# Performance work log

Measured on AMD Instinct MI355X. Metric: run time of the kernel, lower is better.

Reference implementation:

```python
import jax, jax.numpy as jnp
import numpy as np

B, T, C = 64, 384, 256
NH, NKV = 4, 2
HD = C // NH            # 64
NREP = NH // NKV        # 2
NE, TOPK = 8, 2
HID = int(8 / 3 * C)    # 682
EPS_RMS = 1e-6


def _rope_tables(t_len):
    inv_freq = 1.0 / (10000.0 ** (np.arange(0, HD, 2, dtype=np.float32) / HD))
    t = np.arange(t_len, dtype=np.float32)
    freqs = np.outer(t, inv_freq)                      # [T, HD/2]
    emb = np.concatenate([freqs, freqs], axis=-1)      # [T, HD]
    return jnp.asarray(np.cos(emb)), jnp.asarray(np.sin(emb))


def _rotate_half(x):
    h = x.shape[-1] // 2
    return jnp.concatenate([-x[..., h:], x[..., :h]], axis=-1)


def _rmsnorm(v, w):
    return v * jax.lax.rsqrt(jnp.mean(v * v, axis=-1, keepdims=True) + EPS_RMS) * w


def setup_inputs() -> dict:
    key = jax.random.key(0)
    ks = jax.random.split(key, 10)
    s = lambda k, shape: (jax.random.normal(k, shape, jnp.float32) * 0.02)
    return {
        "x": jax.random.normal(ks[0], (B, T, C), jnp.float32),
        "ln1_w": jnp.ones((C,), jnp.float32),
        "ln2_w": jnp.ones((C,), jnp.float32),
        "wq": s(ks[1], (NH * HD, C)),
        "wk": s(ks[2], (NKV * HD, C)),
        "wv": s(ks[3], (NKV * HD, C)),
        "wo": s(ks[4], (C, C)),
        "router_w": s(ks[5], (NE, C)),
        "w1": s(ks[6], (NE, HID, C)),
        "w2": s(ks[7], (NE, C, HID)),
        "w3": s(ks[8], (NE, HID, C)),
    }


def reference(x, ln1_w, ln2_w, wq, wk, wv, wo, router_w, w1, w2, w3):
    Bx, Tx, Cx = x.shape
    # --- attention sub-block ---
    h = _rmsnorm(x, ln1_w)
    q = (h @ wq.T).reshape(Bx, Tx, NH, HD).transpose(0, 2, 1, 3)    # [B,H,T,D]
    k = (h @ wk.T).reshape(Bx, Tx, NKV, HD).transpose(0, 2, 1, 3)   # [B,KV,T,D]
    v = (h @ wv.T).reshape(Bx, Tx, NKV, HD).transpose(0, 2, 1, 3)
    cos, sin = _rope_tables(Tx)
    cos, sin = cos[None, None], sin[None, None]
    q = q * cos + _rotate_half(q) * sin
    k = k * cos + _rotate_half(k) * sin
    k = jnp.repeat(k, NREP, axis=1)   # GQA: expand kv heads
    v = jnp.repeat(v, NREP, axis=1)
    scores = jnp.einsum('bhtd,bhsd->bhts', q, k) / jnp.sqrt(jnp.float32(HD))
    causal = jnp.tril(jnp.ones((Tx, Tx), dtype=bool))
    scores = jnp.where(causal[None, None], scores, jnp.float32(-1e30))
    att = jax.nn.softmax(scores, axis=-1)
    y = jnp.einsum('bhts,bhsd->bhtd', att, v).transpose(0, 2, 1, 3).reshape(Bx, Tx, Cx)
    x = x + y @ wo.T

    # --- MoE sub-block ---
    flat = _rmsnorm(x, ln2_w).reshape(-1, Cx)                  # [N, C]
    probs = jax.nn.softmax(flat @ router_w.T, axis=-1)         # [N, NE]
    tp, ti = jax.lax.top_k(probs, TOPK)
    tp = tp / (jnp.sum(tp, axis=-1, keepdims=True) + 1e-9)
    # per-token per-expert combine weight (0 if not selected)
    weights = jnp.sum(tp[..., None] * jax.nn.one_hot(ti, NE, dtype=flat.dtype), axis=1)  # [N, NE]
    out = jnp.zeros_like(flat)
    for e in range(NE):  # small fixed expert count
        hh = jax.nn.silu(flat @ w1[e].T) * (flat @ w3[e].T)
        out = out + weights[:, e:e + 1] * (hh @ w2[e].T)
    return x + out.reshape(Bx, Tx, Cx)
```

## Files before the change

kernel.cpp:

```cpp
#include <hip/hip_runtime.h>
#include <hip/hip_bf16.h>
#include <math.h>

typedef unsigned short u16t;
typedef __bf16 bf16x8 __attribute__((ext_vector_type(8)));
typedef float f32x4 __attribute__((ext_vector_type(4)));

#define NBATCH 64
#define NT 384
#define NC 256
#define NHID 682
#define NHIDP 704
#define NTOK (NBATCH * NT)
#define NSLOT (2 * NTOK + 1024)

#define SB0 196
#define SB1 (SB0 + 512)
#define SB2 (SB1 + 256)
#define SB3 (SB2 + 5632)
#define SB4 (SB3 + 5632)
#define SB5 (SB4 + 48)
#define SB6 (SB5 + NTOK / 4)

static __device__ __forceinline__ float bf2f(u16t u) { return __uint_as_float(((unsigned int)u) << 16); }
static __device__ __forceinline__ u16t f2bf(float f) { return __builtin_bit_cast(u16t, __float2bfloat16(f)); }

static __device__ __forceinline__ void gload16(const void* gp, void* lp) {
  __builtin_amdgcn_global_load_lds((const __attribute__((address_space(1))) void*)gp,
                                   (__attribute__((address_space(3))) void*)lp, 16, 0, 0);
}

static __device__ __forceinline__ void pipe_barrier_full() {
  asm volatile("s_waitcnt vmcnt(0) lgkmcnt(0)" ::: "memory");
  __builtin_amdgcn_s_barrier();
  asm volatile("" ::: "memory");
}


__global__ __launch_bounds__(256) void k_setup(const float* __restrict__ wq, const float* __restrict__ wk,
                                               const float* __restrict__ wv, const float* __restrict__ wo,
                                               const float* __restrict__ w1, const float* __restrict__ w2,
                                               const float* __restrict__ w3,
                                               const float* __restrict__ x, const float* __restrict__ ln1w,
                                               int* __restrict__ tok, float* __restrict__ tokw,
                                               int* __restrict__ ctrl,
                                               u16t* __restrict__ wqkvb, u16t* __restrict__ wob,
                                               u16t* __restrict__ w1p, u16t* __restrict__ w3p,
                                               u16t* __restrict__ w2p, float* __restrict__ rtab,
                                               u16t* __restrict__ h) {
  int blk = blockIdx.x, t = threadIdx.x;
  if (blk < SB0) {
    int i = blk * 256 + t;
    tok[i] = -1; tokw[i] = 0.f;
    if (blk == 0 && t < 64) ctrl[t] = 0;
  } else if (blk < SB1) {
    int i = (blk - SB0) * 256 + t;
    int row = i >> 8, col = i & 255;
    float s = (row < 256) ? wq[(size_t)row * 256 + col]
            : (row < 384) ? wk[(size_t)(row - 256) * 256 + col]
                          : wv[(size_t)(row - 384) * 256 + col];
    wqkvb[i] = f2bf(s);
  } else if (blk < SB2) {
    int i = (blk - SB1) * 256 + t;
    wob[i] = f2bf(wo[i]);
  } else if (blk < SB3) {
    int idx = (blk - SB2) * 256 + t;
    int kcol = idx & 255; int tmp = idx >> 8; int nrow = tmp % NHIDP; int e = tmp / NHIDP;
    if (nrow < NHID) {
      size_t src = ((size_t)e * NHID + nrow) * NC + kcol;
      w1p[idx] = f2bf(w1[src]); w3p[idx] = f2bf(w3[src]);
    } else { w1p[idx] = 0; w3p[idx] = 0; }
  } else if (blk < SB4) {
    int idx = (blk - SB3) * 256 + t;
    int kcol = idx % NHIDP; int tmp = idx / NHIDP; int nrow = tmp & 255; int e = tmp >> 8;
    w2p[idx] = (kcol < NHID) ? f2bf(w2[((size_t)e * NC + nrow) * NHID + kcol]) : (u16t)0;
  } else if (blk < SB5) {
    int i = (blk - SB4) * 256 + t;
    int tt = i >> 5, d = i & 31;
    float ang = (float)tt * powf(10000.f, -(float)d * (1.f / 32.f));
    float s, c; sincosf(ang, &s, &c);
    ((float2*)rtab)[i] = make_float2(c, s);
  } else {
    int w = t >> 6, l = t & 63;
    int n = (blk - SB5) * 4 + w;
    const float* xr = x + (size_t)n * NC;
    float4 xa = *(const float4*)(xr + l * 4);
    float ssq = xa.x * xa.x + xa.y * xa.y + xa.z * xa.z + xa.w * xa.w;
    for (int d = 1; d < 64; d <<= 1) ssq += __shfl_xor(ssq, d, 64);
    float rs = rsqrtf(ssq * (1.f / 256.f) + 1e-6f);
    float4 wa = *(const float4*)(ln1w + l * 4);
    ushort4 o;
    o.x = f2bf(xa.x * rs * wa.x);
    o.y = f2bf(xa.y * rs * wa.y);
    o.z = f2bf(xa.z * rs * wa.z);
    o.w = f2bf(xa.w * rs * wa.w);
    *(ushort4*)(h + (size_t)n * NC + l * 4) = o;
  }
}

__global__ __launch_bounds__(256) void k_rms_router(const float* __restrict__ xin,
                                                    const float* __restrict__ wg,
                                                    const float* __restrict__ rw,
                                                    u16t* __restrict__ flat,
                                                    int* __restrict__ eidx,
                                                    float* __restrict__ ew) {
  int w = threadIdx.x >> 6, l = threadIdx.x & 63;
  int n = blockIdx.x * 4 + w;
  const float* xr = xin + (size_t)n * NC;
  float4 xa = *(const float4*)(xr + l * 4);
  float ssq = xa.x * xa.x + xa.y * xa.y + xa.z * xa.z + xa.w * xa.w;
  for (int d = 1; d < 64; d <<= 1) ssq += __shfl_xor(ssq, d, 64);
  float rs = rsqrtf(ssq * (1.f / 256.f) + 1e-6f);
  float4 wa = *(const float4*)(wg + l * 4);
  float n0 = xa.x * rs * wa.x, n1 = xa.y * rs * wa.y;
  float n2 = xa.z * rs * wa.z, n3 = xa.w * rs * wa.w;
  ushort4 o; o.x = f2bf(n0); o.y = f2bf(n1); o.z = f2bf(n2); o.w = f2bf(n3);
  *(ushort4*)(flat + (size_t)n * NC + l * 4) = o;
  float acc[8];
  for (int e = 0; e < 8; e++) {
    float4 ra = *(const float4*)(rw + (size_t)e * NC + l * 4);
    acc[e] = n0 * ra.x + n1 * ra.y + n2 * ra.z + n3 * ra.w;
  }
  for (int e = 0; e < 8; e++)
    for (int d = 1; d < 64; d <<= 1) acc[e] += __shfl_xor(acc[e], d, 64);
  if (l == 0) {
    float mx = acc[0];
    for (int e = 1; e < 8; e++) mx = fmaxf(mx, acc[e]);
    float p[8], sum = 0.f;
    for (int e = 0; e < 8; e++) { p[e] = __expf(acc[e] - mx); sum += p[e]; }
    float inv = 1.f / sum;
    for (int e = 0; e < 8; e++) p[e] *= inv;
    int i0 = 0; float b0 = p[0];
    for (int e = 1; e < 8; e++) if (p[e] > b0) { b0 = p[e]; i0 = e; }
    int i1 = -1; float b1 = -1.f;
    for (int e = 0; e < 8; e++) if (e != i0 && p[e] > b1) { b1 = p[e]; i1 = e; }
    float s2 = 1.f / (b0 + b1 + 1e-9f);
    eidx[n * 2] = i0; eidx[n * 2 + 1] = i1;
    ew[n * 2] = b0 * s2; ew[n * 2 + 1] = b1 * s2;
  }
}

__global__ __launch_bounds__(256) void k_hist(const int* __restrict__ eidx, int* __restrict__ ctrl) {
  int* cnt = ctrl; int* offs = ctrl + 8; int* cursor = ctrl + 20; int* done = ctrl + 32;
  __shared__ int lh[8];
  if (threadIdx.x < 8) lh[threadIdx.x] = 0;
  __syncthreads();
  int base = blockIdx.x * 1024 + threadIdx.x;
  for (int i = 0; i < 4; i++) atomicAdd(&lh[eidx[base + i * 256]], 1);
  __syncthreads();
  if (threadIdx.x < 8) {
    atomicAdd(&cnt[threadIdx.x], lh[threadIdx.x]);
    __threadfence();
  }
  __syncthreads();
  if (threadIdx.x == 0) {
    int prev = atomicAdd(done, 1);
    if (prev == 47) {
      int off = 0;
      for (int e = 0; e < 8; e++) {
        int c_ = atomicAdd(&cnt[e], 0);
        offs[e] = off; cursor[e] = off;
        off += ((c_ + 127) >> 7) << 7;
      }
      offs[8] = off;
    }
  }
}

__global__ __launch_bounds__(256) void k_gemm_qkv(const u16t* __restrict__ A,
                                                  const u16t* __restrict__ Bw,
                                                  const float* __restrict__ rtab,
                                                  u16t* __restrict__ qkv) {
  __shared__ __align__(16) u16t sA[2][128 * 64];
  __shared__ __align__(16) u16t sB[2][128 * 64];
  int t = threadIdx.x;
  int m0 = blockIdx.y * 128, n0 = blockIdx.x * 128;
  int w = t >> 6, l = t & 63, quad = l >> 4, lq = l & 15;
  int wm = (w >> 1) * 64, wn = (w & 1) * 64;
  const u16t* aP[4]; const u16t* bP[4];
  for (int i = 0; i < 4; i++) {
    int c = i * 256 + t; int r = c >> 3; int g = (c & 7) ^ (r & 7);
    aP[i] = A + (size_t)(m0 + r) * NC + g * 8;
    bP[i] = Bw + (size_t)(n0 + r) * NC + g * 8;
  }
  auto stage = [&](int p, int k0) {
    for (int i = 0; i < 4; i++) {
      gload16(aP[i] + k0, sA[p] + (size_t)(i * 256 + t) * 8);
      gload16(bP[i] + k0, sB[p] + (size_t)(i * 256 + t) * 8);
    }
  };
  const f32x4 fz = {0.f, 0.f, 0.f, 0.f};
  f32x4 acc[4][4];
  for (int i = 0; i < 4; i++) for (int j = 0; j < 4; j++) acc[i][j] = fz;
  stage(0, 0);
  pipe_barrier_full();
  for (int kb = 0; kb < 4; kb++) {
    int p = kb & 1;
    if (kb < 3) stage(p ^ 1, (kb + 1) << 6);
    for (int kk = 0; kk < 2; kk++) {
      int gq = kk * 4 + quad;
      bf16x8 af[4], bf[4];
      for (int mi = 0; mi < 4; mi++) { int row = wm + mi * 16 + lq; af[mi] = *(const bf16x8*)(sA[p] + (row * 8 + (gq ^ (row & 7))) * 8); }
      for (int ni = 0; ni < 4; ni++) { int row = wn + ni * 16 + lq; bf[ni] = *(const bf16x8*)(sB[p] + (row * 8 + (gq ^ (row & 7))) * 8); }
      for (int mi = 0; mi < 4; mi++)
        for (int ni = 0; ni < 4; ni++)
          acc[mi][ni] = __builtin_amdgcn_mfma_f32_16x16x32_bf16(af[mi], bf[ni], acc[mi][ni], 0, 0, 0);
    }
    if (kb < 3) pipe_barrier_full();
  }
  int cb = (n0 + wn) >> 6;
  const float2* rt = (const float2*)rtab;
  for (int mi = 0; mi < 4; mi++)
    for (int r = 0; r < 4; r++) {
      int gm = m0 + wm + mi * 16 + quad * 4 + r;
      u16t* orow = qkv + (size_t)gm * 512 + n0 + wn;
      if (cb < 6) {
        int tt = gm % NT;
        for (int ni = 0; ni < 2; ni++) {
          int d = ni * 16 + lq;
          float2 cs = rt[tt * 32 + d];
          float x1 = acc[mi][ni][r], x2 = acc[mi][ni + 2][r];
          orow[d] = f2bf(x1 * cs.x - x2 * cs.y);
          orow[d + 32] = f2bf(x2 * cs.x + x1 * cs.y);
        }
      } else {
        for (int ni = 0; ni < 4; ni++) orow[ni * 16 + lq] = f2bf(acc[mi][ni][r]);
      }
    }
}

__global__ __launch_bounds__(256) void k_gemm_wo(const u16t* __restrict__ A,
                                                 const u16t* __restrict__ Bw,
                                                 const float* __restrict__ xin,
                                                 float* __restrict__ xo) {
  __shared__ __align__(16) u16t sA[2][128 * 64];
  __shared__ __align__(16) u16t sB[2][128 * 64];
  int t = threadIdx.x;
  int m0 = blockIdx.y * 128, n0 = blockIdx.x * 128;
  int w = t >> 6, l = t & 63, quad = l >> 4, lq = l & 15;
  int wm = (w >> 1) * 64, wn = (w & 1) * 64;
  const u16t* aP[4]; const u16t* bP[4];
  for (int i = 0; i < 4; i++) {
    int c = i * 256 + t; int r = c >> 3; int g = (c & 7) ^ (r & 7);
    aP[i] = A + (size_t)(m0 + r) * NC + g * 8;
    bP[i] = Bw + (size_t)(n0 + r) * NC + g * 8;
  }
  auto stage = [&](int p, int k0) {
    for (int i = 0; i < 4; i++) {
      gload16(aP[i] + k0, sA[p] + (size_t)(i * 256 + t) * 8);
      gload16(bP[i] + k0, sB[p] + (size_t)(i * 256 + t) * 8);
    }
  };
  const f32x4 fz = {0.f, 0.f, 0.f, 0.f};
  f32x4 acc[4][4];
  for (int i = 0; i < 4; i++) for (int j = 0; j < 4; j++) acc[i][j] = fz;
  stage(0, 0);
  pipe_barrier_full();
  for (int kb = 0; kb < 4; kb++) {
    int p = kb & 1;
    if (kb < 3) stage(p ^ 1, (kb + 1) << 6);
    for (int kk = 0; kk < 2; kk++) {
      int gq = kk * 4 + quad;
      bf16x8 af[4], bf[4];
      for (int mi = 0; mi < 4; mi++) { int row = wm + mi * 16 + lq; af[mi] = *(const bf16x8*)(sA[p] + (row * 8 + (gq ^ (row & 7))) * 8); }
      for (int ni = 0; ni < 4; ni++) { int row = wn + ni * 16 + lq; bf[ni] = *(const bf16x8*)(sB[p] + (row * 8 + (gq ^ (row & 7))) * 8); }
      for (int mi = 0; mi < 4; mi++)
        for (int ni = 0; ni < 4; ni++)
          acc[mi][ni] = __builtin_amdgcn_mfma_f32_16x16x32_bf16(af[mi], bf[ni], acc[mi][ni], 0, 0, 0);
    }
    if (kb < 3) pipe_barrier_full();
  }
  for (int mi = 0; mi < 4; mi++)
    for (int ni = 0; ni < 4; ni++) {
      int gn = n0 + wn + ni * 16 + lq;
      for (int r = 0; r < 4; r++) {
        int gm = m0 + wm + mi * 16 + quad * 4 + r;
        xo[(size_t)gm * NC + gn] = acc[mi][ni][r] + xin[(size_t)gm * NC + gn];
      }
    }
}

__global__ __launch_bounds__(256) void k_attn(const u16t* __restrict__ qkv,
                                              u16t* __restrict__ y) {
  __shared__ __align__(16) u16t sK[2][64 * 64];
  __shared__ __align__(16) u16t sVT[2][64 * 64];
  __shared__ __align__(16) u16t sP[4 * 32 * 64];
  int qt = blockIdx.x, h = blockIdx.y, b = blockIdx.z;
  int kvh = h >> 1;
  int t = threadIdx.x, w = t >> 6, l = t & 63, quad = l >> 4, lq = l & 15;
  int tb = qt * 128 + w * 32;
  bf16x8 qf[2][2];
  for (int mi = 0; mi < 2; mi++)
    for (int kk = 0; kk < 2; kk++)
      qf[mi][kk] = *(const bf16x8*)(qkv + ((size_t)(b * NT + tb + mi * 16 + lq)) * 512 + h * 64 + kk * 32 + quad * 8);
  const f32x4 fz = {0.f, 0.f, 0.f, 0.f};
  f32x4 accO[2][4];
  float mrow[2][4], lrow[2][4];
  for (int mi = 0; mi < 2; mi++)
    for (int ni = 0; ni < 4; ni++) accO[mi][ni] = fz;
  for (int mi = 0; mi < 2; mi++)
    for (int r = 0; r < 4; r++) { mrow[mi][r] = -1e30f; lrow[mi][r] = 0.f; }
  u16t* myP = sP + w * 2048;
  int nkt = (qt + 1) * 2;
  ushort4 vr0[2], vr1[2];
  auto stageK = [&](int p, int kt) {
    int s0 = kt * 64;
    for (int i = 0; i < 2; i++) {
      int c = i * 256 + t; int s = c >> 3; int g = (c & 7) ^ (s & 7);
      gload16(qkv + ((size_t)(b * NT + s0 + s)) * 512 + 256 + kvh * 64 + g * 8, sK[p] + (size_t)c * 8);
    }
  };
  auto vload = [&](int kt) {
    int s0 = kt * 64;
    for (int i = 0; i < 2; i++) {
      int pI = i * 256 + t; int s = pI & 63; int n0 = (pI >> 6) * 8;
      const u16t* vp = qkv + ((size_t)(b * NT + s0 + s)) * 512 + 384 + kvh * 64 + n0;
      vr0[i] = *(const ushort4*)vp; vr1[i] = *(const ushort4*)(vp + 4);
    }
  };
  auto vstore = [&](int p) {
    for (int i = 0; i < 2; i++) {
      int pI = i * 256 + t; int s = pI & 63; int n0 = (pI >> 6) * 8;
      u16t vv[8] = {vr0[i].x, vr0[i].y, vr0[i].z, vr0[i].w, vr1[i].x, vr1[i].y, vr1[i].z, vr1[i].w};
      for (int j = 0; j < 8; j++) {
        int nn = n0 + j;
        sVT[p][(nn * 8 + ((s >> 3) ^ (nn & 7))) * 8 + (s & 7)] = vv[j];
      }
    }
  };
  stageK(0, 0); vload(0); vstore(0);
  pipe_barrier_full();
  for (int kt = 0; kt < nkt; kt++) {
    int p = kt & 1;
    int s0 = kt * 64;
    bool more = (kt + 1 < nkt);
    if (more) { stageK(p ^ 1, kt + 1); vload(kt + 1); }
    if (s0 <= tb + 31) {
      f32x4 accS[2][4];
      for (int mi = 0; mi < 2; mi++) for (int ni = 0; ni < 4; ni++) accS[mi][ni] = fz;
      for (int kk = 0; kk < 2; kk++) {
        int gq = kk * 4 + quad;
        bf16x8 kf[4];
        for (int ni = 0; ni < 4; ni++) { int row = ni * 16 + lq; kf[ni] = *(const bf16x8*)(sK[p] + (row * 8 + (gq ^ (row & 7))) * 8); }
        for (int mi = 0; mi < 2; mi++)
          for (int ni = 0; ni < 4; ni++)
            accS[mi][ni] = __builtin_amdgcn_mfma_f32_16x16x32_bf16(qf[mi][kk], kf[ni], accS[mi][ni], 0, 0, 0);
      }
      for (int mi = 0; mi < 2; mi++) {
        float alpha[4];
        for (int r = 0; r < 4; r++) {
          int trow = tb + mi * 16 + quad * 4 + r;
          float mx = -1e30f;
          for (int ni = 0; ni < 4; ni++) {
            int ss = s0 + ni * 16 + lq;
            float sv = accS[mi][ni][r] * 0.125f;
            sv = (ss > trow) ? -1e30f : sv;
            accS[mi][ni][r] = sv;
            mx = fmaxf(mx, sv);
          }
          for (int d = 1; d < 16; d <<= 1) mx = fmaxf(mx, __shfl_xor(mx, d, 64));
          float mnew = fmaxf(mrow[mi][r], mx);
          float al = __expf(mrow[mi][r] - mnew);
          float rsum = 0.f;
          for (int ni = 0; ni < 4; ni++) {
            float p2 = __expf(accS[mi][ni][r] - mnew);
            accS[mi][ni][r] = p2;
            rsum += p2;
          }
          for (int d = 1; d < 16; d <<= 1) rsum += __shfl_xor(rsum, d, 64);
          lrow[mi][r] = lrow[mi][r] * al + rsum;
          mrow[mi][r] = mnew;
          alpha[r] = al;
        }
        for (int ni = 0; ni < 4; ni++)
          for (int r = 0; r < 4; r++) accO[mi][ni][r] *= alpha[r];
        for (int ni = 0; ni < 4; ni++) {
          int cc = ni * 16 + lq;
          for (int r = 0; r < 4; r++) {
            int row = mi * 16 + quad * 4 + r;
            myP[((cc >> 3) * 32 + row) * 8 + (cc & 7)] = f2bf(accS[mi][ni][r]);
          }
        }
      }
      asm volatile("s_waitcnt lgkmcnt(0)" ::: "memory");
      for (int kk = 0; kk < 2; kk++) {
        int gq = kk * 4 + quad;
        bf16x8 pf[2], vf[4];
        for (int mi = 0; mi < 2; mi++) { int row = mi * 16 + lq; pf[mi] = *(const bf16x8*)(myP + (gq * 32 + row) * 8); }
        for (int ni = 0; ni < 4; ni++) { int row = ni * 16 + lq; vf[ni] = *(const bf16x8*)(sVT[p] + (row * 8 + (gq ^ (row & 7))) * 8); }
        for (int mi = 0; mi < 2; mi++)
          for (int ni = 0; ni < 4; ni++)
            accO[mi][ni] = __builtin_amdgcn_mfma_f32_16x16x32_bf16(pf[mi], vf[ni], accO[mi][ni], 0, 0, 0);
      }
    }
    if (more) {
      vstore(p ^ 1);
      pipe_barrier_full();
    }
  }
  for (int mi = 0; mi < 2; mi++)
    for (int r = 0; r < 4; r++) {
      int trow = tb + mi * 16 + quad * 4 + r;
      float inv = 1.f / lrow[mi][r];
      for (int ni = 0; ni < 4; ni++) {
        int d = ni * 16 + lq;
        y[((size_t)(b * NT + trow)) * NC + h * 64 + d] = f2bf(accO[mi][ni][r] * inv);
      }
    }
}

__global__ __launch_bounds__(256) void k_scatter(const int* __restrict__ eidx, const float* __restrict__ ew,
                                                 int* __restrict__ cursor, int* __restrict__ tok,
                                                 float* __restrict__ tokw, int* __restrict__ t2s) {
  __shared__ int lcnt[8], lbase[8];
  if (threadIdx.x < 8) lcnt[threadIdx.x] = 0;
  __syncthreads();
  int n = blockIdx.x * 256 + threadIdx.x;
  int e0 = eidx[n * 2], e1 = eidx[n * 2 + 1];
  int p0 = atomicAdd(&lcnt[e0], 1);
  int p1 = atomicAdd(&lcnt[e1], 1);
  __syncthreads();
  if (threadIdx.x < 8) lbase[threadIdx.x] = atomicAdd(&cursor[threadIdx.x], lcnt[threadIdx.x]);
  __syncthreads();
  int g0 = lbase[e0] + p0, g1 = lbase[e1] + p1;
  tok[g0] = n; tokw[g0] = ew[n * 2];
  tok[g1] = n; tokw[g1] = ew[n * 2 + 1];
  t2s[n * 2] = g0; t2s[n * 2 + 1] = g1;
}

__global__ __launch_bounds__(256) void k_moe_e1(const u16t* __restrict__ flat,
                                                const u16t* __restrict__ w1p,
                                                const u16t* __restrict__ w3p,
                                                const int* __restrict__ offs,
                                                const int* __restrict__ tok,
                                                u16t* __restrict__ hh) {
  __shared__ __align__(16) u16t sA[128 * 64];
  __shared__ __align__(16) u16t sB1[64 * 64];
  __shared__ __align__(16) u16t sB3[64 * 64];
  int t = threadIdx.x;
  int bid = blockIdx.x;
  int work = (bid & 7) * 539 + (bid >> 3);
  int sb = work / 11;
  int slot0 = sb * 128, n0 = (work - sb * 11) * 64;
  int e = 7;
  for (int i = 0; i < 8; i++) { if (slot0 < offs[i + 1]) { e = i; break; } }
  const u16t* B1 = w1p + (size_t)e * NHIDP * NC;
  const u16t* B3 = w3p + (size_t)e * NHIDP * NC;
  int w = t >> 6, l = t & 63, quad = l >> 4, lq = l & 15;
  int wm = (w >> 1) * 64, wn = (w & 1) * 32;
  const u16t* aP[4]; const u16t* b1P[2]; const u16t* b3P[2];
  for (int i = 0; i < 4; i++) {
    int c = i * 256 + t; int r = c >> 3; int g = (c & 7) ^ (r & 7);
    int tk = tok[slot0 + r]; int row = (tk < 0) ? 0 : tk;
    aP[i] = flat + (size_t)row * NC + g * 8;
  }
  for (int i = 0; i < 2; i++) {
    int c = i * 256 + t; int r = c >> 3; int g = (c & 7) ^ (r & 7);
    b1P[i] = B1 + (size_t)(n0 + r) * NC + g * 8;
    b3P[i] = B3 + (size_t)(n0 + r) * NC + g * 8;
  }
  const f32x4 fz = {0.f, 0.f, 0.f, 0.f};
  f32x4 a1[4][2], a3[4][2];
  for (int i = 0; i < 4; i++) for (int j = 0; j < 2; j++) { a1[i][j] = fz; a3[i][j] = fz; }
  for (int kb = 0; kb < 4; kb++) {
    int k0 = kb << 6;
    for (int i = 0; i < 4; i++)
      gload16(aP[i] + k0, sA + (size_t)(i * 256 + t) * 8);
    for (int i = 0; i < 2; i++) {
      gload16(b1P[i] + k0, sB1 + (size_t)(i * 256 + t) * 8);
      gload16(b3P[i] + k0, sB3 + (size_t)(i * 256 + t) * 8);
    }
    __syncthreads();
    for (int kk = 0; kk < 2; kk++) {
      int gq = kk * 4 + quad;
      bf16x8 af[4], b1f[2], b3f[2];
      for (int mi = 0; mi < 4; mi++) { int row = wm + mi * 16 + lq; af[mi] = *(const bf16x8*)(sA + (row * 8 + (gq ^ (row & 7))) * 8); }
      for (int ni = 0; ni < 2; ni++) {
        int row = wn + ni * 16 + lq;
        b1f[ni] = *(const bf16x8*)(sB1 + (row * 8 + (gq ^ (row & 7))) * 8);
        b3f[ni] = *(const bf16x8*)(sB3 + (row * 8 + (gq ^ (row & 7))) * 8);
      }
      for (int mi = 0; mi < 4; mi++)
        for (int ni = 0; ni < 2; ni++) {
          a1[mi][ni] = __builtin_amdgcn_mfma_f32_16x16x32_bf16(af[mi], b1f[ni], a1[mi][ni], 0, 0, 0);
          a3[mi][ni] = __builtin_amdgcn_mfma_f32_16x16x32_bf16(af[mi], b3f[ni], a3[mi][ni], 0, 0, 0);
        }
    }
    __syncthreads();
  }
  for (int mi = 0; mi < 4; mi++)
    for (int ni = 0; ni < 2; ni++) {
      int gn = n0 + wn + ni * 16 + lq;
      for (int r = 0; r < 4; r++) {
        int slot = slot0 + wm + mi * 16 + quad * 4 + r;
        float v1 = a1[mi][ni][r], v3 = a3[mi][ni][r];
        float hv = v1 / (1.f + __expf(-v1)) * v3;
        hh[(size_t)slot * NHIDP + gn] = f2bf(hv);
      }
    }
}

__global__ __launch_bounds__(256) void k_moe_e2(const u16t* __restrict__ hh,
                                                const u16t* __restrict__ w2p,
                                                const int* __restrict__ offs,
                                                const float* __restrict__ tokw,
                                                u16t* __restrict__ eo) {
  __shared__ __align__(16) u16t sA[128 * 64];
  __shared__ __align__(16) u16t sB[128 * 64];
  int t = threadIdx.x;
  int bid = blockIdx.x;
  int work = (bid & 7) * 98 + (bid >> 3);
  int slot0 = (work >> 1) * 128, n0 = (work & 1) * 128;
  int e = 7;
  for (int i = 0; i < 8; i++) { if (slot0 < offs[i + 1]) { e = i; break; } }
  const u16t* Bw = w2p + (size_t)e * NC * NHIDP;
  int w = t >> 6, l = t & 63, quad = l >> 4, lq = l & 15;
  int wm = (w >> 1) * 64, wn = (w & 1) * 64;
  const u16t* aP[4]; const u16t* bP[4];
  for (int i = 0; i < 4; i++) {
    int c = i * 256 + t; int r = c >> 3; int g = (c & 7) ^ (r & 7);
    aP[i] = hh + (size_t)(slot0 + r) * NHIDP + g * 8;
    bP[i] = Bw + (size_t)(n0 + r) * NHIDP + g * 8;
  }
  const f32x4 fz = {0.f, 0.f, 0.f, 0.f};
  f32x4 acc[4][4];
  for (int i = 0; i < 4; i++) for (int j = 0; j < 4; j++) acc[i][j] = fz;
  for (int kb = 0; kb < 11; kb++) {
    int k0 = kb << 6;
    for (int i = 0; i < 4; i++) {
      gload16(aP[i] + k0, sA + (size_t)(i * 256 + t) * 8);
      gload16(bP[i] + k0, sB + (size_t)(i * 256 + t) * 8);
    }
    __syncthreads();
    for (int kk = 0; kk < 2; kk++) {
      int gq = kk * 4 + quad;
      bf16x8 af[4], bf[4];
      for (int mi = 0; mi < 4; mi++) { int row = wm + mi * 16 + lq; af[mi] = *(const bf16x8*)(sA + (row * 8 + (gq ^ (row & 7))) * 8); }
      for (int ni = 0; ni < 4; ni++) { int row = wn + ni * 16 + lq; bf[ni] = *(const bf16x8*)(sB + (row * 8 + (gq ^ (row & 7))) * 8); }
      for (int mi = 0; mi < 4; mi++)
        for (int ni = 0; ni < 4; ni++)
          acc[mi][ni] = __builtin_amdgcn_mfma_f32_16x16x32_bf16(af[mi], bf[ni], acc[mi][ni], 0, 0, 0);
    }
    __syncthreads();
  }
  for (int mi = 0; mi < 4; mi++)
    for (int r = 0; r < 4; r++) {
      int slot = slot0 + wm + mi * 16 + quad * 4 + r;
      float wgt = tokw[slot];
      for (int ni = 0; ni < 4; ni++) {
        int gn = n0 + wn + ni * 16 + lq;
        eo[(size_t)slot * NC + gn] = f2bf(wgt * acc[mi][ni][r]);
      }
    }
}

__global__ __launch_bounds__(256) void k_combine(const u16t* __restrict__ eo,
                                                 const int* __restrict__ t2s,
                                                 float* __restrict__ xo) {
  int w = threadIdx.x >> 6, l = threadIdx.x & 63;
  int n = blockIdx.x * 4 + w;
  int g0 = t2s[n * 2], g1 = t2s[n * 2 + 1];
  float* xr = xo + (size_t)n * NC + l * 4;
  float4 xa = *(const float4*)xr;
  ushort4 a = *(const ushort4*)(eo + (size_t)g0 * NC + l * 4);
  ushort4 b = *(const ushort4*)(eo + (size_t)g1 * NC + l * 4);
  xa.x += bf2f(a.x) + bf2f(b.x);
  xa.y += bf2f(a.y) + bf2f(b.y);
  xa.z += bf2f(a.z) + bf2f(b.z);
  xa.w += bf2f(a.w) + bf2f(b.w);
  *(float4*)xr = xa;
}

extern "C" void kernel_launch(void* const* d_in, const int* in_sizes, int n_in,
                              void* d_out, int out_size, void* d_ws, size_t ws_size,
                              hipStream_t stream) {
  (void)in_sizes; (void)n_in; (void)out_size; (void)ws_size;
  const float* x    = (const float*)d_in[0];
  const float* ln1w = (const float*)d_in[1];
  const float* ln2w = (const float*)d_in[2];
  const float* wq   = (const float*)d_in[3];
  const float* wk   = (const float*)d_in[4];
  const float* wv   = (const float*)d_in[5];
  const float* wo   = (const float*)d_in[6];
  const float* rw   = (const float*)d_in[7];
  const float* w1   = (const float*)d_in[8];
  const float* w2   = (const float*)d_in[9];
  const float* w3   = (const float*)d_in[10];
  float* xo = (float*)d_out;

  char* ws = (char*)d_ws;
  size_t off = 0;
  int* ctrl  = (int*)(ws + off);  off += 4096;
  int* eidx  = (int*)(ws + off);  off += (size_t)NTOK * 2 * 4;
  float* ew  = (float*)(ws + off); off += (size_t)NTOK * 2 * 4;
  int* tok   = (int*)(ws + off);  off += (size_t)NSLOT * 4;
  float* tokw = (float*)(ws + off); off += (size_t)NSLOT * 4;
  int* t2s   = (int*)(ws + off);  off += (size_t)NTOK * 2 * 4;
  u16t* wqkvb = (u16t*)(ws + off); off += (size_t)512 * 256 * 2;
  u16t* wob  = (u16t*)(ws + off); off += (size_t)256 * 256 * 2;
  u16t* w1p  = (u16t*)(ws + off); off += (size_t)8 * NHIDP * NC * 2;
  u16t* w3p  = (u16t*)(ws + off); off += (size_t)8 * NHIDP * NC * 2;
  u16t* w2p  = (u16t*)(ws + off); off += (size_t)8 * NC * NHIDP * 2;
  float* rtab = (float*)(ws + off); off += (size_t)NT * 32 * 2 * 4;
  u16t* h    = (u16t*)(ws + off); off += (size_t)NTOK * NC * 2;
  u16t* qkv  = (u16t*)(ws + off); off += (size_t)NTOK * 512 * 2;
  u16t* y    = (u16t*)(ws + off); off += (size_t)NTOK * NC * 2;
  u16t* flat = (u16t*)(ws + off); off += (size_t)NTOK * NC * 2;
  u16t* hh   = (u16t*)(ws + off); off += (size_t)NSLOT * NHIDP * 2;
  u16t* eo   = h;
  int* offs = ctrl + 8; int* cursor = ctrl + 20;

  k_setup<<<SB6, 256, 0, stream>>>(wq, wk, wv, wo, w1, w2, w3, x, ln1w,
                                   tok, tokw, ctrl, wqkvb, wob, w1p, w3p, w2p, rtab, h);
  k_gemm_qkv<<<dim3(4, NTOK / 128), 256, 0, stream>>>(h, wqkvb, rtab, qkv);
  k_attn<<<dim3(3, 4, NBATCH), 256, 0, stream>>>(qkv, y);
  k_gemm_wo<<<dim3(2, NTOK / 128), 256, 0, stream>>>(y, wob, x, xo);

  k_rms_router<<<NTOK / 4, 256, 0, stream>>>(xo, ln2w, rw, flat, eidx, ew);
  k_hist<<<48, 256, 0, stream>>>(eidx, ctrl);
  k_scatter<<<NTOK / 256, 256, 0, stream>>>(eidx, ew, cursor, tok, tokw, t2s);
  k_moe_e1<<<4312, 256, 0, stream>>>(flat, w1p, w3p, offs, tok, hh);
  k_moe_e2<<<784, 256, 0, stream>>>(hh, w2p, offs, tokw, eo);
  k_combine<<<NTOK / 4, 256, 0, stream>>>(eo, t2s, xo);
}
```

Measured before the change: 297.8 us.

## Fuse histogram and scatter via grid flag; widen MoE expert-1 tiles to 128 columns

The separate histogram and scatter kernels become one kernel of 96 blocks. The last block to finish computes the expert offsets, and every block spin-waits on a global flag before scattering tokens, which saves one launch. The first MoE GEMM now uses 512-thread blocks with 128-column tiles of w1/w3. The hidden dimension is padded to 768 so it divides evenly, which halves the block count and reuses each A tile across more columns. The spin-wait relies on all 96 blocks being co-resident, and the padded columns add some wasted MFMA work.

```diff
diff --git a/kernel.cpp b/kernel.cpp
--- a/kernel.cpp
+++ b/kernel.cpp
@@ -11,13 +11,14 @@
 #define NC 256
 #define NHID 682
 #define NHIDP 704
+#define NHIDR 768
 #define NTOK (NBATCH * NT)
 #define NSLOT (2 * NTOK + 1024)
 
 #define SB0 196
 #define SB1 (SB0 + 512)
 #define SB2 (SB1 + 256)
-#define SB3 (SB2 + 5632)
+#define SB3 (SB2 + 6144)
 #define SB4 (SB3 + 5632)
 #define SB5 (SB4 + 48)
 #define SB6 (SB5 + NTOK / 4)
@@ -65,7 +66,7 @@
     wob[i] = f2bf(wo[i]);
   } else if (blk < SB3) {
     int idx = (blk - SB2) * 256 + t;
-    int kcol = idx & 255; int tmp = idx >> 8; int nrow = tmp % NHIDP; int e = tmp / NHIDP;
+    int kcol = idx & 255; int tmp = idx >> 8; int nrow = tmp % NHIDR; int e = tmp / NHIDR;
     if (nrow < NHID) {
       size_t src = ((size_t)e * NHID + nrow) * NC + kcol;
       w1p[idx] = f2bf(w1[src]); w3p[idx] = f2bf(w3[src]);
@@ -140,31 +141,50 @@
   }
 }
 
-__global__ __launch_bounds__(256) void k_hist(const int* __restrict__ eidx, int* __restrict__ ctrl) {
-  int* cnt = ctrl; int* offs = ctrl + 8; int* cursor = ctrl + 20; int* done = ctrl + 32;
-  __shared__ int lh[8];
-  if (threadIdx.x < 8) lh[threadIdx.x] = 0;
+__global__ __launch_bounds__(256) void k_hist_scatter(const int* __restrict__ eidx, const float* __restrict__ ew,
+                                                      int* __restrict__ ctrl, int* __restrict__ tok,
+                                                      float* __restrict__ tokw, int* __restrict__ t2s) {
+  int* cnt = ctrl; int* offs = ctrl + 8; int* cursor = ctrl + 20;
+  int* done = ctrl + 32; int* flag = ctrl + 33;
+  __shared__ int lh[8], lcnt[8], lbase[8];
+  int tid = threadIdx.x;
+  if (tid < 8) { lh[tid] = 0; lcnt[tid] = 0; }
   __syncthreads();
-  int base = blockIdx.x * 1024 + threadIdx.x;
-  for (int i = 0; i < 4; i++) atomicAdd(&lh[eidx[base + i * 256]], 1);
+  int n = blockIdx.x * 256 + tid;
+  int e0 = eidx[n * 2], e1 = eidx[n * 2 + 1];
+  atomicAdd(&lh[e0], 1); atomicAdd(&lh[e1], 1);
   __syncthreads();
-  if (threadIdx.x < 8) {
-    atomicAdd(&cnt[threadIdx.x], lh[threadIdx.x]);
+  if (tid < 8) {
+    atomicAdd(&cnt[tid], lh[tid]);
     __threadfence();
   }
   __syncthreads();
-  if (threadIdx.x == 0) {
+  if (tid == 0) {
     int prev = atomicAdd(done, 1);
-    if (prev == 47) {
+    if (prev == 95) {
       int off = 0;
       for (int e = 0; e < 8; e++) {
         int c_ = atomicAdd(&cnt[e], 0);
-        offs[e] = off; cursor[e] = off;
+        offs[e] = off;
+        atomicExch(&cursor[e], off);
         off += ((c_ + 127) >> 7) << 7;
       }
       offs[8] = off;
-    }
-  }
+      __threadfence();
+      atomicExch(flag, 1);
+    }
+    while (atomicAdd(flag, 0) == 0) {}
+  }
+  __syncthreads();
+  int p0 = atomicAdd(&lcnt[e0], 1);
+  int p1 = atomicAdd(&lcnt[e1], 1);
+  __syncthreads();
+  if (tid < 8) lbase[tid] = atomicAdd(&cursor[tid], lcnt[tid]);
+  __syncthreads();
+  int g0 = lbase[e0] + p0, g1 = lbase[e1] + p1;
+  tok[g0] = n; tokw[g0] = ew[n * 2];
+  tok[g1] = n; tokw[g1] = ew[n * 2 + 1];
+  t2s[n * 2] = g0; t2s[n * 2 + 1] = g1;
 }
 
 __global__ __launch_bounds__(256) void k_gemm_qkv(const u16t* __restrict__ A,
@@ -409,53 +429,31 @@
     }
 }
 
-__global__ __launch_bounds__(256) void k_scatter(const int* __restrict__ eidx, const float* __restrict__ ew,
-                                                 int* __restrict__ cursor, int* __restrict__ tok,
-                                                 float* __restrict__ tokw, int* __restrict__ t2s) {
-  __shared__ int lcnt[8], lbase[8];
-  if (threadIdx.x < 8) lcnt[threadIdx.x] = 0;
-  __syncthreads();
-  int n = blockIdx.x * 256 + threadIdx.x;
-  int e0 = eidx[n * 2], e1 = eidx[n * 2 + 1];
-  int p0 = atomicAdd(&lcnt[e0], 1);
-  int p1 = atomicAdd(&lcnt[e1], 1);
-  __syncthreads();
-  if (threadIdx.x < 8) lbase[threadIdx.x] = atomicAdd(&cursor[threadIdx.x], lcnt[threadIdx.x]);
-  __syncthreads();
-  int g0 = lbase[e0] + p0, g1 = lbase[e1] + p1;
-  tok[g0] = n; tokw[g0] = ew[n * 2];
-  tok[g1] = n; tokw[g1] = ew[n * 2 + 1];
-  t2s[n * 2] = g0; t2s[n * 2 + 1] = g1;
-}
-
-__global__ __launch_bounds__(256) void k_moe_e1(const u16t* __restrict__ flat,
+__global__ __launch_bounds__(512) void k_moe_e1(const u16t* __restrict__ flat,
                                                 const u16t* __restrict__ w1p,
                                                 const u16t* __restrict__ w3p,
                                                 const int* __restrict__ offs,
                                                 const int* __restrict__ tok,
                                                 u16t* __restrict__ hh) {
   __shared__ __align__(16) u16t sA[128 * 64];
-  __shared__ __align__(16) u16t sB1[64 * 64];
-  __shared__ __align__(16) u16t sB3[64 * 64];
+  __shared__ __align__(16) u16t sB1[128 * 64];
+  __shared__ __align__(16) u16t sB3[128 * 64];
   int t = threadIdx.x;
   int bid = blockIdx.x;
-  int work = (bid & 7) * 539 + (bid >> 3);
-  int sb = work / 11;
-  int slot0 = sb * 128, n0 = (work - sb * 11) * 64;
+  int work = (bid & 7) * 294 + (bid >> 3);
+  int sb = work / 6;
+  int slot0 = sb * 128, n0 = (work - sb * 6) * 128;
   int e = 7;
   for (int i = 0; i < 8; i++) { if (slot0 < offs[i + 1]) { e = i; break; } }
-  const u16t* B1 = w1p + (size_t)e * NHIDP * NC;
-  const u16t* B3 = w3p + (size_t)e * NHIDP * NC;
+  const u16t* B1 = w1p + (size_t)e * NHIDR * NC;
+  const u16t* B3 = w3p + (size_t)e * NHIDR * NC;
   int w = t >> 6, l = t & 63, quad = l >> 4, lq = l & 15;
-  int wm = (w >> 1) * 64, wn = (w & 1) * 32;
-  const u16t* aP[4]; const u16t* b1P[2]; const u16t* b3P[2];
-  for (int i = 0; i < 4; i++) {
-    int c = i * 256 + t; int r = c >> 3; int g = (c & 7) ^ (r & 7);
+  int wm = (w >> 2) * 64, wn = (w & 3) * 32;
+  const u16t* aP[2]; const u16t* b1P[2]; const u16t* b3P[2];
+  for (int i = 0; i < 2; i++) {
+    int c = i * 512 + t; int r = c >> 3; int g = (c & 7) ^ (r & 7);
     int tk = tok[slot0 + r]; int row = (tk < 0) ? 0 : tk;
     aP[i] = flat + (size_t)row * NC + g * 8;
-  }
-  for (int i = 0; i < 2; i++) {
-    int c = i * 256 + t; int r = c >> 3; int g = (c & 7) ^ (r & 7);
     b1P[i] = B1 + (size_t)(n0 + r) * NC + g * 8;
     b3P[i] = B3 + (size_t)(n0 + r) * NC + g * 8;
   }
@@ -464,11 +462,10 @@
   for (int i = 0; i < 4; i++) for (int j = 0; j < 2; j++) { a1[i][j] = fz; a3[i][j] = fz; }
   for (int kb = 0; kb < 4; kb++) {
     int k0 = kb << 6;
-    for (int i = 0; i < 4; i++)
-      gload16(aP[i] + k0, sA + (size_t)(i * 256 + t) * 8);
     for (int i = 0; i < 2; i++) {
-      gload16(b1P[i] + k0, sB1 + (size_t)(i * 256 + t) * 8);
-      gload16(b3P[i] + k0, sB3 + (size_t)(i * 256 + t) * 8);
+      gload16(aP[i] + k0, sA + (size_t)(i * 512 + t) * 8);
+      gload16(b1P[i] + k0, sB1 + (size_t)(i * 512 + t) * 8);
+      gload16(b3P[i] + k0, sB3 + (size_t)(i * 512 + t) * 8);
     }
     __syncthreads();
     for (int kk = 0; kk < 2; kk++) {
@@ -491,11 +488,13 @@
   for (int mi = 0; mi < 4; mi++)
     for (int ni = 0; ni < 2; ni++) {
       int gn = n0 + wn + ni * 16 + lq;
-      for (int r = 0; r < 4; r++) {
-        int slot = slot0 + wm + mi * 16 + quad * 4 + r;
-        float v1 = a1[mi][ni][r], v3 = a3[mi][ni][r];
-        float hv = v1 / (1.f + __expf(-v1)) * v3;
-        hh[(size_t)slot * NHIDP + gn] = f2bf(hv);
+      if (gn < NHIDP) {
+        for (int r = 0; r < 4; r++) {
+          int slot = slot0 + wm + mi * 16 + quad * 4 + r;
+          float v1 = a1[mi][ni][r], v3 = a3[mi][ni][r];
+          float hv = v1 / (1.f + __expf(-v1)) * v3;
+          hh[(size_t)slot * NHIDP + gn] = f2bf(hv);
+        }
       }
     }
 }
@@ -598,8 +597,8 @@
   int* t2s   = (int*)(ws + off);  off += (size_t)NTOK * 2 * 4;
   u16t* wqkvb = (u16t*)(ws + off); off += (size_t)512 * 256 * 2;
   u16t* wob  = (u16t*)(ws + off); off += (size_t)256 * 256 * 2;
-  u16t* w1p  = (u16t*)(ws + off); off += (size_t)8 * NHIDP * NC * 2;
-  u16t* w3p  = (u16t*)(ws + off); off += (size_t)8 * NHIDP * NC * 2;
+  u16t* w1p  = (u16t*)(ws + off); off += (size_t)8 * NHIDR * NC * 2;
+  u16t* w3p  = (u16t*)(ws + off); off += (size_t)8 * NHIDR * NC * 2;
   u16t* w2p  = (u16t*)(ws + off); off += (size_t)8 * NC * NHIDP * 2;
   float* rtab = (float*)(ws + off); off += (size_t)NT * 32 * 2 * 4;
   u16t* h    = (u16t*)(ws + off); off += (size_t)NTOK * NC * 2;
@@ -608,7 +607,7 @@
   u16t* flat = (u16t*)(ws + off); off += (size_t)NTOK * NC * 2;
   u16t* hh   = (u16t*)(ws + off); off += (size_t)NSLOT * NHIDP * 2;
   u16t* eo   = h;
-  int* offs = ctrl + 8; int* cursor = ctrl + 20;
+  int* offs = ctrl + 8;
 
   k_setup<<<SB6, 256, 0, stream>>>(wq, wk, wv, wo, w1, w2, w3, x, ln1w,
                                    tok, tokw, ctrl, wqkvb, wob, w1p, w3p, w2p, rtab, h);
@@ -617,9 +616,8 @@
   k_gemm_wo<<<dim3(2, NTOK / 128), 256, 0, stream>>>(y, wob, x, xo);
 
   k_rms_router<<<NTOK / 4, 256, 0, stream>>>(xo, ln2w, rw, flat, eidx, ew);
-  k_hist<<<48, 256, 0, stream>>>(eidx, ctrl);
-  k_scatter<<<NTOK / 256, 256, 0, stream>>>(eidx, ew, cursor, tok, tokw, t2s);
-  k_moe_e1<<<4312, 256, 0, stream>>>(flat, w1p, w3p, offs, tok, hh);
+  k_hist_scatter<<<NTOK / 256, 256, 0, stream>>>(eidx, ew, ctrl, tok, tokw, t2s);
+  k_moe_e1<<<2352, 512, 0, stream>>>(flat, w1p, w3p, offs, tok, hh);
   k_moe_e2<<<784, 256, 0, stream>>>(hh, w2p, offs, tokw, eo);
   k_combine<<<NTOK / 4, 256, 0, stream>>>(eo, t2s, xo);
 }
```

Measured after the change: 308.6 us. 1.04x slower.
